# Optimization experiments

Measured on AMD Instinct MI355X. Metric: run time of the kernel, lower is better.

The kernel has to match this reference:

```python
import jax, jax.numpy as jnp
import numpy as np

N = 50000      # nodes
E = 400000     # edges (before self-loops)
IN = 128       # in_channels
H = 4          # heads
C = 64         # hidden_channels == out_channels (per head)
ELI = 200000   # link-prediction query edges
NEG_SLOPE = 0.2
EPS = 1e-5


def setup_inputs():
    key = jax.random.key(0)
    ks = jax.random.split(key, 20)
    sc = 0.05
    inp = {}
    inp["x"] = jax.random.normal(ks[0], (N, IN), jnp.float32)
    inp["edge_index"] = jax.random.randint(ks[1], (2, E), 0, N)
    inp["edge_label_index"] = jax.random.randint(ks[2], (2, ELI), 0, N)
    # layer 1 GATv2 params
    inp["Wl1"] = jax.random.normal(ks[3], (IN, H * C), jnp.float32) * sc
    inp["bl1"] = jnp.zeros((H * C,), jnp.float32)
    inp["Wr1"] = jax.random.normal(ks[4], (IN, H * C), jnp.float32) * sc
    inp["br1"] = jnp.zeros((H * C,), jnp.float32)
    inp["att1"] = jax.random.normal(ks[5], (H, C), jnp.float32) * sc
    inp["bias1"] = jnp.zeros((C,), jnp.float32)
    # norm1 (BatchNorm affine)
    inp["g1"] = jnp.ones((C,), jnp.float32)
    inp["b1"] = jnp.zeros((C,), jnp.float32)
    # residual projection 1 (in_channels 128 -> hidden_dim 64)
    inp["Wres"] = jax.random.normal(ks[6], (IN, C), jnp.float32) * sc
    inp["bres"] = jnp.zeros((C,), jnp.float32)
    # layer 2 GATv2 params (hidden_dim 64 -> out 64)
    inp["Wl2"] = jax.random.normal(ks[7], (C, H * C), jnp.float32) * sc
    inp["bl2"] = jnp.zeros((H * C,), jnp.float32)
    inp["Wr2"] = jax.random.normal(ks[8], (C, H * C), jnp.float32) * sc
    inp["br2"] = jnp.zeros((H * C,), jnp.float32)
    inp["att2"] = jax.random.normal(ks[9], (H, C), jnp.float32) * sc
    inp["bias2"] = jnp.zeros((C,), jnp.float32)
    # norm2
    inp["g2"] = jnp.ones((C,), jnp.float32)
    inp["b2"] = jnp.zeros((C,), jnp.float32)
    return inp


def _gatv2(x, src, dst, Wl, bl, Wr, br, att, bias, n):
    # PyG GATv2Conv, concat=False (mean over heads), dropout off (eval)
    xl = (x @ Wl + bl).reshape(n, H, -1)   # source transform
    xr = (x @ Wr + br).reshape(n, H, -1)   # target transform
    e = jax.nn.leaky_relu(xl[src] + xr[dst], NEG_SLOPE)      # [E,H,C]
    logits = jnp.einsum('ehc,hc->eh', e, att)                # [E,H]
    m = jax.ops.segment_max(logits, dst, num_segments=n)     # segment softmax
    p = jnp.exp(logits - m[dst])
    s = jax.ops.segment_sum(p, dst, num_segments=n)
    alpha = p / s[dst]                                       # [E,H]
    out = jax.ops.segment_sum(xl[src] * alpha[:, :, None], dst, num_segments=n)
    return out.mean(axis=1) + bias                           # [N,C]


def _bn(x, g, b):
    mu = x.mean(axis=0)
    var = x.var(axis=0)
    return g * (x - mu) * jax.lax.rsqrt(var + EPS) + b


def reference(x, edge_index, edge_label_index,
              Wl1, bl1, Wr1, br1, att1, bias1, g1, b1, Wres, bres,
              Wl2, bl2, Wr2, br2, att2, bias2, g2, b2):
    loop = jnp.arange(N)
    src = jnp.concatenate([edge_index[0], loop])  # add_self_loops=True
    dst = jnp.concatenate([edge_index[1], loop])
    x_res = x @ Wres + bres
    h = _gatv2(x, src, dst, Wl1, bl1, Wr1, br1, att1, bias1, N)
    h = jax.nn.relu(_bn(h, g1, b1) + x_res)
    # res_proj2 is Identity (hidden_dim == out_dim)
    h2 = _gatv2(h, src, dst, Wl2, bl2, Wr2, br2, att2, bias2, N)
    z = _bn(h2, g2, b2) + h
    scores = (z[edge_label_index[0]] * z[edge_label_index[1]]).sum(axis=-1)
    return jax.nn.sigmoid(scores)
```

## Files before the change

kernel.cpp:

```cpp
#include <hip/hip_runtime.h>
#include <math.h>

#define NN 50000
#define EE 400000
#define ETOT 450000
#define INC 128
#define CC 64
#define HC 256
#define ELI_N 200000
#define MPAD 50176
#define GB1 1800
#define FILLB ((ETOT + 255) / 256)

typedef unsigned short u16;
typedef __attribute__((ext_vector_type(8))) short short8v;
typedef __attribute__((ext_vector_type(8))) unsigned short u16x8;
typedef __attribute__((ext_vector_type(4))) float f32x4;
typedef __attribute__((ext_vector_type(4))) unsigned short u16x4;

__device__ __forceinline__ u16 f2b(float v){
    unsigned u = __float_as_uint(v);
    u = (u + 0x7fffu + ((u >> 16) & 1u)) >> 16;
    return (u16)u;
}
__device__ __forceinline__ float b2f(u16 h){
    return __uint_as_float(((unsigned)h) << 16);
}
__device__ __forceinline__ u16 f2h(float v){
    _Float16 h = (_Float16)v; u16 r; __builtin_memcpy(&r, &h, 2); return r;
}
__device__ __forceinline__ float h2f(u16 h){
    _Float16 x; __builtin_memcpy(&x, &h, 2); return (float)x;
}
__device__ __forceinline__ f32x4 h2f4(u16x4 r){
    f32x4 o; o[0]=h2f(r[0]); o[1]=h2f(r[1]); o[2]=h2f(r[2]); o[3]=h2f(r[3]); return o;
}

__global__ void k_setup(const float* __restrict__ x, const int* __restrict__ ei,
                        const float* __restrict__ Wl1, const float* __restrict__ Wr1,
                        const float* __restrict__ Wres, const float* __restrict__ Wl2,
                        const float* __restrict__ Wr2,
                        u16* __restrict__ xhi, u16* __restrict__ xlo,
                        u16* __restrict__ hl1, u16* __restrict__ ll1,
                        u16* __restrict__ hr1, u16* __restrict__ lr1,
                        u16* __restrict__ hres, u16* __restrict__ lres,
                        u16* __restrict__ hl2, u16* __restrict__ ll2,
                        u16* __restrict__ hr2, u16* __restrict__ lr2,
                        int* __restrict__ deg){
    int gid = blockIdx.x*256 + threadIdx.x;
    if (gid < 800000){
        int row = gid >> 4;
        int k0  = (gid & 15) * 8;
        const float* ap = x + (size_t)row*128 + k0;
        float4 v0 = *(const float4*)ap;
        float4 v1 = *(const float4*)(ap + 4);
        float vv[8] = {v0.x, v0.y, v0.z, v0.w, v1.x, v1.y, v1.z, v1.w};
        u16x8 h8, l8;
        #pragma unroll
        for (int j = 0; j < 8; j++){
            u16 h = f2b(vv[j]);
            h8[j] = h;
            l8[j] = f2b(vv[j] - b2f(h));
        }
        size_t blk = (size_t)(row >> 4)*4 + (k0 >> 5);
        size_t addr = blk*512 + (size_t)((row & 15) + 16*((k0 >> 3) & 3))*8;
        *(u16x8*)(xhi + addr) = h8;
        *(u16x8*)(xlo + addr) = l8;
    } else if (gid < 906496){
        int g = gid - 800000;
        const float* src; u16* dh; u16* dl; int K, N, idx;
        if      (g <  32768){ src=Wl1;  dh=hl1;  dl=ll1;  K=128; N=256; idx=g; }
        else if (g <  65536){ src=Wr1;  dh=hr1;  dl=lr1;  K=128; N=256; idx=g-32768; }
        else if (g <  73728){ src=Wres; dh=hres; dl=lres; K=128; N=64;  idx=g-65536; }
        else if (g <  90112){ src=Wl2;  dh=hl2;  dl=ll2;  K=64;  N=256; idx=g-73728; }
        else                { src=Wr2;  dh=hr2;  dl=lr2;  K=64;  N=256; idx=g-90112; }
        int k = idx / N, n = idx - k*N;
        float v = src[idx];
        u16 h = f2b(v);
        size_t blk = (size_t)(n >> 4)*(K >> 5) + (k >> 5);
        size_t addr = blk*512 + (size_t)((n & 15) + 16*((k >> 3) & 3))*8 + (k & 7);
        dh[addr] = h;
        dl[addr] = f2b(v - b2f(h));
    } else if (gid < 1306496){
        int e = gid - 906496;
        atomicAdd(&deg[ei[EE + e]], 1);
    }
}

__global__ void k_scanA(const int* __restrict__ deg, int* __restrict__ iscan, int* __restrict__ part){
    __shared__ int sh[256];
    int tid = threadIdx.x;
    int base = blockIdx.x*1024 + tid*4;
    int v[4]; int t = 0;
    #pragma unroll
    for (int i = 0; i < 4; i++){ int idx = base + i; v[i] = (idx < NN) ? deg[idx]+1 : 0; t += v[i]; }
    sh[tid] = t; __syncthreads();
    for (int off = 1; off < 256; off <<= 1){
        int u = (tid >= off) ? sh[tid - off] : 0;
        __syncthreads();
        sh[tid] += u;
        __syncthreads();
    }
    int incl = sh[tid];
    int run = incl - t;
    #pragma unroll
    for (int i = 0; i < 4; i++){
        run += v[i];
        int idx = base + i;
        if (idx < NN) iscan[idx] = run;
    }
    if (tid == 255) part[blockIdx.x] = incl;
}

__global__ void k_scanC(const int* __restrict__ iscan, const int* __restrict__ part,
                        const int* __restrict__ deg, int* __restrict__ rowptr, int* __restrict__ cursor){
    int chunk = blockIdx.x >> 2;
    int ps = 0;
    for (int j = 0; j < chunk; j++) ps += part[j];
    int i = blockIdx.x*256 + threadIdx.x;
    if (i < NN){
        int v = iscan[i] + ps;
        rowptr[i+1] = v;
        cursor[i] = v - (deg[i]+1);
    }
    if (i == 0) rowptr[0] = 0;
}

__global__ __launch_bounds__(256) void k_gemm1(const u16* __restrict__ Ahi, const u16* __restrict__ Alo,
        const u16* __restrict__ Whl1, const u16* __restrict__ Wll1,
        const u16* __restrict__ Whr1, const u16* __restrict__ Wlr1,
        const u16* __restrict__ Whres,const u16* __restrict__ Wlres,
        const float* __restrict__ bl1, const float* __restrict__ br1, const float* __restrict__ bres,
        u16* __restrict__ xl, u16* __restrict__ xr, float* __restrict__ xres,
        const int* __restrict__ ei, int* __restrict__ cursor, int* __restrict__ csr_src)
{
    int b = blockIdx.x;
    if (b >= GB1){
        int idx = (b - GB1)*256 + threadIdx.x;
        if (idx < ETOT){
            int s, d;
            if (idx < EE){ s = ei[idx]; d = ei[EE + idx]; }
            else         { s = idx - EE; d = s; }
            int pos = atomicAdd(&cursor[d], 1);
            csr_src[pos] = s;
        }
        return;
    }
    int c = b & 7;
    int k = b >> 3;
    int tile = k % 9;
    int sx = c + 8*(k/9);
    if (sx >= 196) return;
    int wid = threadIdx.x >> 6, lane = threadIdx.x & 63;
    const u16 *Bh, *Bl; const float* bias; int n0;
    u16* C16 = 0; float* C32 = 0;
    if (tile < 4)      { Bh=Whl1;  Bl=Wll1;  bias=bl1;  C16=xl;   n0=tile*64; }
    else if (tile < 8) { Bh=Whr1;  Bl=Wlr1;  bias=br1;  C16=xr;   n0=(tile-4)*64; }
    else               { Bh=Whres; Bl=Wlres; bias=bres; C32=xres; n0=0; }
    int rm0 = (sx*4 + wid) * 64;
    int rblk0 = rm0 >> 4;
    int nblk0 = n0 >> 4;
    int lr = lane & 15;
    f32x4 acc[4][4] = {};
    #pragma unroll
    for (int ks = 0; ks < 4; ks++){
        short8v ah[4], al[4], bh[4], blo[4];
        #pragma unroll
        for (int mf = 0; mf < 4; mf++){
            size_t addr = ((size_t)(rblk0 + mf)*4 + ks)*512 + (size_t)lane*8;
            ah[mf] = *(const short8v*)(Ahi + addr);
            al[mf] = *(const short8v*)(Alo + addr);
        }
        #pragma unroll
        for (int nf = 0; nf < 4; nf++){
            size_t addr = ((size_t)(nblk0 + nf)*4 + ks)*512 + (size_t)lane*8;
            bh[nf]  = *(const short8v*)(Bh + addr);
            blo[nf] = *(const short8v*)(Bl + addr);
        }
        #pragma unroll
        for (int mf = 0; mf < 4; mf++)
            #pragma unroll
            for (int nf = 0; nf < 4; nf++){
                acc[mf][nf] = __builtin_amdgcn_mfma_f32_16x16x32_bf16(ah[mf], bh[nf],  acc[mf][nf], 0, 0, 0);
                acc[mf][nf] = __builtin_amdgcn_mfma_f32_16x16x32_bf16(al[mf], bh[nf],  acc[mf][nf], 0, 0, 0);
                acc[mf][nf] = __builtin_amdgcn_mfma_f32_16x16x32_bf16(ah[mf], blo[nf], acc[mf][nf], 0, 0, 0);
            }
    }
    int rbase = (lane >> 4) << 2;
    #pragma unroll
    for (int nf = 0; nf < 4; nf++){
        int col = n0 + nf*16 + lr;
        float bv = bias[col];
        #pragma unroll
        for (int mf = 0; mf < 4; mf++){
            #pragma unroll
            for (int r = 0; r < 4; r++){
                int row = rm0 + mf*16 + rbase + r;
                if (row < NN){
                    float v = acc[mf][nf][r] + bv;
                    if (tile < 8) C16[(size_t)row*256 + col] = f2h(v);
                    else          C32[(size_t)row*64  + col] = v;
                }
            }
        }
    }
}

__global__ __launch_bounds__(256) void k_gemm2(const u16* __restrict__ Ahi, const u16* __restrict__ Alo,
        const u16* __restrict__ Whl2, const u16* __restrict__ Wll2,
        const u16* __restrict__ Whr2, const u16* __restrict__ Wlr2,
        const float* __restrict__ bl2, const float* __restrict__ br2,
        u16* __restrict__ xl, u16* __restrict__ xr)
{
    int b = blockIdx.x;
    int c = b & 7;
    int k = b >> 3;
    int tile = k & 7;
    int sx = c + 8*(k >> 3);
    if (sx >= 196) return;
    int wid = threadIdx.x >> 6, lane = threadIdx.x & 63;
    const u16 *Bh, *Bl; const float* bias; u16* Cout;
    if (tile < 4){ Bh=Whl2; Bl=Wll2; bias=bl2; Cout=xl; }
    else         { Bh=Whr2; Bl=Wlr2; bias=br2; Cout=xr; }
    int n0 = (tile & 3)*64;
    int rm0 = (sx*4 + wid) * 64;
    int rblk0 = rm0 >> 4;
    int nblk0 = n0 >> 4;
    int lr = lane & 15;
    f32x4 acc[4][4] = {};
    #pragma unroll
    for (int ks = 0; ks < 2; ks++){
        short8v ah[4], al[4], bh[4], blo[4];
        #pragma unroll
        for (int mf = 0; mf < 4; mf++){
            size_t addr = ((size_t)(rblk0 + mf)*2 + ks)*512 + (size_t)lane*8;
            ah[mf] = *(const short8v*)(Ahi + addr);
            al[mf] = *(const short8v*)(Alo + addr);
        }
        #pragma unroll
        for (int nf = 0; nf < 4; nf++){
            size_t addr = ((size_t)(nblk0 + nf)*2 + ks)*512 + (size_t)lane*8;
            bh[nf]  = *(const short8v*)(Bh + addr);
            blo[nf] = *(const short8v*)(Bl + addr);
        }
        #pragma unroll
        for (int mf = 0; mf < 4; mf++)
            #pragma unroll
            for (int nf = 0; nf < 4; nf++){
                acc[mf][nf] = __builtin_amdgcn_mfma_f32_16x16x32_bf16(ah[mf], bh[nf],  acc[mf][nf], 0, 0, 0);
                acc[mf][nf] = __builtin_amdgcn_mfma_f32_16x16x32_bf16(al[mf], bh[nf],  acc[mf][nf], 0, 0, 0);
                acc[mf][nf] = __builtin_amdgcn_mfma_f32_16x16x32_bf16(ah[mf], blo[nf], acc[mf][nf], 0, 0, 0);
            }
    }
    int rbase = (lane >> 4) << 2;
    #pragma unroll
    for (int nf = 0; nf < 4; nf++){
        int col = n0 + nf*16 + lr;
        float bv = bias[col];
        #pragma unroll
        for (int mf = 0; mf < 4; mf++){
            #pragma unroll
            for (int r = 0; r < 4; r++){
                int row = rm0 + mf*16 + rbase + r;
                if (row < NN) Cout[(size_t)row*256 + col] = f2h(acc[mf][nf][r] + bv);
            }
        }
    }
}

__global__ __launch_bounds__(256) void k_gat(const u16* __restrict__ xl, const u16* __restrict__ xr,
                                             const int* __restrict__ csr_src, const int* __restrict__ rowptr,
                                             const float* __restrict__ att, const float* __restrict__ bias,
                                             float* __restrict__ out,
                                             float* __restrict__ part_s, float* __restrict__ part_q)
{
    __shared__ float ls[4][64];
    __shared__ float lq[4][64];
    int wave = threadIdx.x >> 6, lane = threadIdx.x & 63;
    int node = blockIdx.x*4 + wave;
    int p0 = rowptr[node], p1 = rowptr[node+1];
    f32x4 xrf  = h2f4(*(const u16x4*)(xr + (size_t)node*HC + 4*lane));
    f32x4 attf = *(const f32x4*)(att + 4*lane);
    float s = 0.f;
    f32x4 acc = {0.f, 0.f, 0.f, 0.f};
    int p = p0;
    for (; p + 4 <= p1; p += 4){
        int i0 = csr_src[p], i1 = csr_src[p+1], i2 = csr_src[p+2], i3 = csr_src[p+3];
        f32x4 x0 = h2f4(*(const u16x4*)(xl + (size_t)i0*HC + 4*lane));
        f32x4 x1 = h2f4(*(const u16x4*)(xl + (size_t)i1*HC + 4*lane));
        f32x4 x2 = h2f4(*(const u16x4*)(xl + (size_t)i2*HC + 4*lane));
        f32x4 x3 = h2f4(*(const u16x4*)(xl + (size_t)i3*HC + 4*lane));
        float t0 = 0.f, t1 = 0.f, t2 = 0.f, t3 = 0.f;
        #pragma unroll
        for (int j = 0; j < 4; j++){
            float e0 = x0[j] + xrf[j]; e0 = (e0 > 0.f) ? e0 : 0.2f*e0; t0 += e0*attf[j];
            float e1 = x1[j] + xrf[j]; e1 = (e1 > 0.f) ? e1 : 0.2f*e1; t1 += e1*attf[j];
            float e2 = x2[j] + xrf[j]; e2 = (e2 > 0.f) ? e2 : 0.2f*e2; t2 += e2*attf[j];
            float e3 = x3[j] + xrf[j]; e3 = (e3 > 0.f) ? e3 : 0.2f*e3; t3 += e3*attf[j];
        }
        #pragma unroll
        for (int off = 1; off < 16; off <<= 1){
            t0 += __shfl_xor(t0, off, 64);
            t1 += __shfl_xor(t1, off, 64);
            t2 += __shfl_xor(t2, off, 64);
            t3 += __shfl_xor(t3, off, 64);
        }
        float w0 = __expf(t0), w1 = __expf(t1), w2 = __expf(t2), w3 = __expf(t3);
        s += (w0 + w1) + (w2 + w3);
        acc = acc + x0*w0 + x1*w1 + x2*w2 + x3*w3;
    }
    for (; p < p1; p++){
        int i0 = csr_src[p];
        f32x4 x0 = h2f4(*(const u16x4*)(xl + (size_t)i0*HC + 4*lane));
        float t0 = 0.f;
        #pragma unroll
        for (int j = 0; j < 4; j++){ float e0 = x0[j] + xrf[j]; e0 = (e0 > 0.f) ? e0 : 0.2f*e0; t0 += e0*attf[j]; }
        #pragma unroll
        for (int off = 1; off < 16; off <<= 1) t0 += __shfl_xor(t0, off, 64);
        float w0 = __expf(t0);
        s += w0;
        acc = acc + x0*w0;
    }
    float inv = 1.f / s;
    f32x4 o = acc * inv;
    #pragma unroll
    for (int j = 0; j < 4; j++){ o[j] += __shfl_xor(o[j], 16, 64); o[j] += __shfl_xor(o[j], 32, 64); }
    if (lane < 16){
        f32x4 bv = *(const f32x4*)(bias + 4*lane);
        f32x4 res = o*0.25f + bv;
        *(f32x4*)(out + (size_t)node*CC + 4*lane) = res;
        #pragma unroll
        for (int j = 0; j < 4; j++){
            ls[wave][4*lane + j] = res[j];
            lq[wave][4*lane + j] = res[j]*res[j];
        }
    }
    __syncthreads();
    int tid = threadIdx.x;
    if (tid < 128){
        int c = tid & 63;
        if (tid < 64){
            float v = (ls[0][c] + ls[1][c]) + (ls[2][c] + ls[3][c]);
            atomicAdd(&part_s[(blockIdx.x & 63)*64 + c], v);
        } else {
            float v = (lq[0][c] + lq[1][c]) + (lq[2][c] + lq[3][c]);
            atomicAdd(&part_q[(blockIdx.x & 63)*64 + c], v);
        }
    }
}

__global__ __launch_bounds__(256) void k_post1(const float* __restrict__ hraw, const float* __restrict__ xres,
                        const float* __restrict__ part_s, const float* __restrict__ part_q,
                        const float* __restrict__ g, const float* __restrict__ b,
                        float* __restrict__ out, u16* __restrict__ hhi, u16* __restrict__ hlo){
    __shared__ float red[128];
    int tid = threadIdx.x;
    if (tid < 128){
        const float* base = (tid < 64) ? part_s : part_q;
        int c = tid & 63;
        float sv = 0.f;
        for (int bb = 0; bb < 64; bb++) sv += base[bb*64 + c];
        red[tid] = sv;
    }
    __syncthreads();
    int i = blockIdx.x*256 + tid;
    if (i >= NN*16) return;
    float4 hv = ((const float4*)hraw)[i];
    float4 rv = ((const float4*)xres)[i];
    int row = i >> 4;
    int c0 = (i & 15) * 4;
    float hp[4] = {hv.x, hv.y, hv.z, hv.w};
    float rp[4] = {rv.x, rv.y, rv.z, rv.w};
    float res[4];
    u16x4 h4, l4;
    const float invN = 1.f / (float)NN;
    #pragma unroll
    for (int k = 0; k < 4; k++){
        int c = c0 + k;
        float mean = red[c] * invN;
        float var  = red[64 + c] * invN - mean*mean;
        float rstd = rsqrtf(var + 1e-5f);
        float v = g[c]*(hp[k] - mean)*rstd + b[c] + rp[k];
        v = (v > 0.f) ? v : 0.f;
        res[k] = v;
        u16 h = f2b(v);
        h4[k] = h;
        l4[k] = f2b(v - b2f(h));
    }
    ((float4*)out)[i] = make_float4(res[0], res[1], res[2], res[3]);
    size_t blk = (size_t)(row >> 4)*2 + (c0 >> 5);
    size_t addr = blk*512 + (size_t)((row & 15) + 16*((c0 >> 3) & 3))*8 + (c0 & 7);
    *(u16x4*)(hhi + addr) = h4;
    *(u16x4*)(hlo + addr) = l4;
}

__global__ __launch_bounds__(256) void k_post2(const float* __restrict__ hraw, const float* __restrict__ hprev,
                        const float* __restrict__ part_s, const float* __restrict__ part_q,
                        const float* __restrict__ g, const float* __restrict__ b,
                        u16* __restrict__ zout){
    __shared__ float red[128];
    int tid = threadIdx.x;
    if (tid < 128){
        const float* base = (tid < 64) ? part_s : part_q;
        int c = tid & 63;
        float sv = 0.f;
        for (int bb = 0; bb < 64; bb++) sv += base[bb*64 + c];
        red[tid] = sv;
    }
    __syncthreads();
    int i = blockIdx.x*256 + tid;
    if (i >= NN*16) return;
    float4 hv = ((const float4*)hraw)[i];
    float4 rv = ((const float4*)hprev)[i];
    int c0 = (i & 15) * 4;
    float hp[4] = {hv.x, hv.y, hv.z, hv.w};
    float rp[4] = {rv.x, rv.y, rv.z, rv.w};
    u16x4 res;
    const float invN = 1.f / (float)NN;
    #pragma unroll
    for (int k = 0; k < 4; k++){
        int c = c0 + k;
        float mean = red[c] * invN;
        float var  = red[64 + c] * invN - mean*mean;
        float rstd = rsqrtf(var + 1e-5f);
        res[k] = f2h(g[c]*(hp[k] - mean)*rstd + b[c] + rp[k]);
    }
    *(u16x4*)(zout + (size_t)i*4) = res;
}

__global__ __launch_bounds__(256) void k_score(const u16* __restrict__ z, const int* __restrict__ eli,
                                               float* __restrict__ out){
    int t = blockIdx.x*256 + threadIdx.x;
    int i = t >> 4; int j = t & 15;
    if (i >= ELI_N) return;
    int a = eli[i], b = eli[ELI_N + i];
    f32x4 va = h2f4(*(const u16x4*)(z + (size_t)a*64 + j*4));
    f32x4 vb = h2f4(*(const u16x4*)(z + (size_t)b*64 + j*4));
    float s = va[0]*vb[0] + va[1]*vb[1] + va[2]*vb[2] + va[3]*vb[3];
    #pragma unroll
    for (int off = 8; off > 0; off >>= 1) s += __shfl_xor(s, off, 64);
    if (j == 0) out[i] = 1.f / (1.f + __expf(-s));
}

extern "C" void kernel_launch(void* const* d_in, const int* in_sizes, int n_in,
                              void* d_out, int out_size, void* d_ws, size_t ws_size,
                              hipStream_t stream) {
    const float* x    = (const float*)d_in[0];
    const int*   ei   = (const int*)  d_in[1];
    const int*   eli  = (const int*)  d_in[2];
    const float* Wl1  = (const float*)d_in[3];
    const float* bl1  = (const float*)d_in[4];
    const float* Wr1  = (const float*)d_in[5];
    const float* br1  = (const float*)d_in[6];
    const float* att1 = (const float*)d_in[7];
    const float* bias1= (const float*)d_in[8];
    const float* g1   = (const float*)d_in[9];
    const float* b1   = (const float*)d_in[10];
    const float* Wres = (const float*)d_in[11];
    const float* bres = (const float*)d_in[12];
    const float* Wl2  = (const float*)d_in[13];
    const float* bl2  = (const float*)d_in[14];
    const float* Wr2  = (const float*)d_in[15];
    const float* br2  = (const float*)d_in[16];
    const float* att2 = (const float*)d_in[17];
    const float* bias2= (const float*)d_in[18];
    const float* g2   = (const float*)d_in[19];
    const float* b2   = (const float*)d_in[20];
    float* out = (float*)d_out;

    char* w = (char*)d_ws;
    size_t o = 0;
    auto take = [&](size_t bytes)->char*{ char* p = w + o; o += (bytes + 255) & ~(size_t)255; return p; };
    u16*  xl   = (u16*) take((size_t)NN*HC*2);
    u16*  xr   = (u16*) take((size_t)NN*HC*2);
    float* xres = (float*)take((size_t)NN*CC*4);
    float* hraw = (float*)take((size_t)NN*CC*4);
    float* hbuf = (float*)take((size_t)NN*CC*4);
    u16*  z16  = (u16*) take((size_t)NN*CC*2);
    u16*  xhi  = (u16*)take((size_t)MPAD*INC*2);
    u16*  xlo  = (u16*)take((size_t)MPAD*INC*2);
    u16*  hhi  = (u16*)take((size_t)MPAD*CC*2);
    u16*  hlo  = (u16*)take((size_t)MPAD*CC*2);
    u16* whl1 = (u16*)take(256*128*2);  u16* wll1 = (u16*)take(256*128*2);
    u16* whr1 = (u16*)take(256*128*2);  u16* wlr1 = (u16*)take(256*128*2);
    u16* whres= (u16*)take(64*128*2);   u16* wlres= (u16*)take(64*128*2);
    u16* whl2 = (u16*)take(256*64*2);   u16* wll2 = (u16*)take(256*64*2);
    u16* whr2 = (u16*)take(256*64*2);   u16* wlr2 = (u16*)take(256*64*2);
    char* zreg  = take(4*64*64*4 + (size_t)NN*4);
    float* ps1  = (float*)zreg;
    float* pq1  = ps1 + 4096;
    float* ps2  = ps1 + 8192;
    float* pq2  = ps1 + 12288;
    int* deg    = (int*)(zreg + 4*64*64*4);
    int* rowptr = (int*)take((size_t)(NN+1)*4);
    int* iscan  = (int*)take((size_t)NN*4);
    int* cursor = (int*)take((size_t)NN*4);
    int* csr_src= (int*)take((size_t)ETOT*4);
    int* part   = (int*)take(64*4);

    hipMemsetAsync(zreg, 0, 4*64*64*4 + (size_t)NN*4, stream);

    k_setup<<<5104, 256, 0, stream>>>(x, ei, Wl1, Wr1, Wres, Wl2, Wr2,
                                      xhi, xlo,
                                      whl1, wll1, whr1, wlr1, whres, wlres,
                                      whl2, wll2, whr2, wlr2, deg);

    k_scanA<<<49, 256, 0, stream>>>(deg, iscan, part);
    k_scanC<<<196, 256, 0, stream>>>(iscan, part, deg, rowptr, cursor);

    k_gemm1<<<GB1 + FILLB, 256, 0, stream>>>(xhi, xlo, whl1, wll1, whr1, wlr1, whres, wlres,
                                             bl1, br1, bres, xl, xr, xres,
                                             ei, cursor, csr_src);
    k_gat<<<NN/4, 256, 0, stream>>>(xl, xr, csr_src, rowptr, att1, bias1, hraw, ps1, pq1);
    k_post1<<<(NN*16+255)/256, 256, 0, stream>>>(hraw, xres, ps1, pq1, g1, b1, hbuf, hhi, hlo);

    k_gemm2<<<1600, 256, 0, stream>>>(hhi, hlo, whl2, wll2, whr2, wlr2, bl2, br2, xl, xr);
    k_gat<<<NN/4, 256, 0, stream>>>(xl, xr, csr_src, rowptr, att2, bias2, hraw, ps2, pq2);
    k_post2<<<(NN*16+255)/256, 256, 0, stream>>>(hraw, hbuf, ps2, pq2, g2, b2, z16);

    k_score<<<(ELI_N*16+255)/256, 256, 0, stream>>>(z16, eli, out);
}
```

Baseline: 291.6 us.

## Split CSR fill into its own kernel and store residual projection in fp16

Moves the CSR edge-scatter out of the fused gemm1 launch into a separate k_fill kernel, so the gemm blocks no longer share a grid with the atomic scatter blocks. It also writes the residual projection xres as fp16 instead of fp32, which halves its write traffic in gemm1 and its read traffic in post1. The cost is an extra kernel launch and the loss of overlap between the scatter and the GEMM, plus reduced precision in the residual path.

```diff
diff --git a/kernel.cpp b/kernel.cpp
--- a/kernel.cpp
+++ b/kernel.cpp
@@ -9,8 +9,6 @@
 #define HC 256
 #define ELI_N 200000
 #define MPAD 50176
-#define GB1 1800
-#define FILLB ((ETOT + 255) / 256)
 
 typedef unsigned short u16;
 typedef __attribute__((ext_vector_type(8))) short short8v;
@@ -126,37 +124,34 @@
     if (i == 0) rowptr[0] = 0;
 }
 
+__global__ void k_fill(const int* __restrict__ ei, int* __restrict__ cursor, int* __restrict__ csr_src){
+    int idx = blockIdx.x*256 + threadIdx.x;
+    if (idx >= ETOT) return;
+    int s, d;
+    if (idx < EE){ s = ei[idx]; d = ei[EE + idx]; }
+    else         { s = idx - EE; d = s; }
+    int pos = atomicAdd(&cursor[d], 1);
+    csr_src[pos] = s;
+}
+
 __global__ __launch_bounds__(256) void k_gemm1(const u16* __restrict__ Ahi, const u16* __restrict__ Alo,
         const u16* __restrict__ Whl1, const u16* __restrict__ Wll1,
         const u16* __restrict__ Whr1, const u16* __restrict__ Wlr1,
         const u16* __restrict__ Whres,const u16* __restrict__ Wlres,
         const float* __restrict__ bl1, const float* __restrict__ br1, const float* __restrict__ bres,
-        u16* __restrict__ xl, u16* __restrict__ xr, float* __restrict__ xres,
-        const int* __restrict__ ei, int* __restrict__ cursor, int* __restrict__ csr_src)
+        u16* __restrict__ xl, u16* __restrict__ xr, u16* __restrict__ xres)
 {
     int b = blockIdx.x;
-    if (b >= GB1){
-        int idx = (b - GB1)*256 + threadIdx.x;
-        if (idx < ETOT){
-            int s, d;
-            if (idx < EE){ s = ei[idx]; d = ei[EE + idx]; }
-            else         { s = idx - EE; d = s; }
-            int pos = atomicAdd(&cursor[d], 1);
-            csr_src[pos] = s;
-        }
-        return;
-    }
     int c = b & 7;
     int k = b >> 3;
     int tile = k % 9;
     int sx = c + 8*(k/9);
     if (sx >= 196) return;
     int wid = threadIdx.x >> 6, lane = threadIdx.x & 63;
-    const u16 *Bh, *Bl; const float* bias; int n0;
-    u16* C16 = 0; float* C32 = 0;
-    if (tile < 4)      { Bh=Whl1;  Bl=Wll1;  bias=bl1;  C16=xl;   n0=tile*64; }
-    else if (tile < 8) { Bh=Whr1;  Bl=Wlr1;  bias=br1;  C16=xr;   n0=(tile-4)*64; }
-    else               { Bh=Whres; Bl=Wlres; bias=bres; C32=xres; n0=0; }
+    const u16 *Bh, *Bl; const float* bias; u16* Cout; int n0, N;
+    if (tile < 4)      { Bh=Whl1;  Bl=Wll1;  bias=bl1;  Cout=xl;   n0=tile*64;     N=256; }
+    else if (tile < 8) { Bh=Whr1;  Bl=Wlr1;  bias=br1;  Cout=xr;   n0=(tile-4)*64; N=256; }
+    else               { Bh=Whres; Bl=Wlres; bias=bres; Cout=xres; n0=0;           N=64;  }
     int rm0 = (sx*4 + wid) * 64;
     int rblk0 = rm0 >> 4;
     int nblk0 = n0 >> 4;
@@ -196,11 +191,7 @@
             #pragma unroll
             for (int r = 0; r < 4; r++){
                 int row = rm0 + mf*16 + rbase + r;
-                if (row < NN){
-                    float v = acc[mf][nf][r] + bv;
-                    if (tile < 8) C16[(size_t)row*256 + col] = f2h(v);
-                    else          C32[(size_t)row*64  + col] = v;
-                }
+                if (row < NN) Cout[(size_t)row*N + col] = f2h(acc[mf][nf][r] + bv);
             }
         }
     }
@@ -349,7 +340,7 @@
     }
 }
 
-__global__ __launch_bounds__(256) void k_post1(const float* __restrict__ hraw, const float* __restrict__ xres,
+__global__ __launch_bounds__(256) void k_post1(const float* __restrict__ hraw, const u16* __restrict__ xres,
                         const float* __restrict__ part_s, const float* __restrict__ part_q,
                         const float* __restrict__ g, const float* __restrict__ b,
                         float* __restrict__ out, u16* __restrict__ hhi, u16* __restrict__ hlo){
@@ -366,11 +357,10 @@
     int i = blockIdx.x*256 + tid;
     if (i >= NN*16) return;
     float4 hv = ((const float4*)hraw)[i];
-    float4 rv = ((const float4*)xres)[i];
+    f32x4 rp = h2f4(*(const u16x4*)(xres + (size_t)i*4));
     int row = i >> 4;
     int c0 = (i & 15) * 4;
     float hp[4] = {hv.x, hv.y, hv.z, hv.w};
-    float rp[4] = {rv.x, rv.y, rv.z, rv.w};
     float res[4];
     u16x4 h4, l4;
     const float invN = 1.f / (float)NN;
@@ -473,7 +463,7 @@
     auto take = [&](size_t bytes)->char*{ char* p = w + o; o += (bytes + 255) & ~(size_t)255; return p; };
     u16*  xl   = (u16*) take((size_t)NN*HC*2);
     u16*  xr   = (u16*) take((size_t)NN*HC*2);
-    float* xres = (float*)take((size_t)NN*CC*4);
+    u16*  xres = (u16*) take((size_t)NN*CC*2);
     float* hraw = (float*)take((size_t)NN*CC*4);
     float* hbuf = (float*)take((size_t)NN*CC*4);
     u16*  z16  = (u16*) take((size_t)NN*CC*2);
@@ -507,10 +497,10 @@
 
     k_scanA<<<49, 256, 0, stream>>>(deg, iscan, part);
     k_scanC<<<196, 256, 0, stream>>>(iscan, part, deg, rowptr, cursor);
-
-    k_gemm1<<<GB1 + FILLB, 256, 0, stream>>>(xhi, xlo, whl1, wll1, whr1, wlr1, whres, wlres,
-                                             bl1, br1, bres, xl, xr, xres,
-                                             ei, cursor, csr_src);
+    k_fill<<<(ETOT+255)/256, 256, 0, stream>>>(ei, cursor, csr_src);
+
+    k_gemm1<<<1800, 256, 0, stream>>>(xhi, xlo, whl1, wll1, whr1, wlr1, whres, wlres,
+                                      bl1, br1, bres, xl, xr, xres);
     k_gat<<<NN/4, 256, 0, stream>>>(xl, xr, csr_src, rowptr, att1, bias1, hraw, ps1, pq1);
     k_post1<<<(NN*16+255)/256, 256, 0, stream>>>(hraw, xres, ps1, pq1, g1, b1, hbuf, hhi, hlo);
 
```

Result: no change. 289.1 us (-0.9%).
